# Kernel tuning notes

Measured on AMD Instinct MI355X. Metric: run time of the kernel, lower is better.

Reference implementation:

```python
import jax, jax.numpy as jnp
import numpy as np

T, H, E, K, I, S = 512, 1024, 32, 4, 512, 2048  # tokens, hidden, experts, top_k, moe_inter, shared_inter


def setup_inputs() -> dict:
    key = jax.random.key(0)
    ks = jax.random.split(key, 8)
    sc = 0.02
    return {
        "hidden_states": jax.random.normal(ks[0], (T, H), jnp.float32),
        "Wg": jax.random.normal(ks[1], (H, E + 1), jnp.float32) * sc,          # router gate + shared gate (merged)
        "W_gate": jax.random.normal(ks[2], (E, H, I), jnp.float32) * sc,        # per-expert gate proj
        "W_up": jax.random.normal(ks[3], (E, H, I), jnp.float32) * sc,          # per-expert up proj
        "W_down": jax.random.normal(ks[4], (E, I, H), jnp.float32) * sc,        # per-expert down proj
        "Ws_gate": jax.random.normal(ks[5], (H, S), jnp.float32) * sc,          # shared expert gate proj
        "Ws_up": jax.random.normal(ks[6], (H, S), jnp.float32) * sc,            # shared expert up proj
        "Ws_down": jax.random.normal(ks[7], (S, H), jnp.float32) * sc,          # shared expert down proj
    }


def reference(hidden_states, Wg, W_gate, W_up, W_down, Ws_gate, Ws_up, Ws_down):
    x = hidden_states  # [T, H]
    logits = x @ Wg                       # [T, E+1]
    router_logits = logits[:, :E]         # [T, E]
    shared_gate_logits = logits[:, E:]    # [T, 1]

    # top-k softmax routing with renormalization (renormalize=True)
    probs = jax.nn.softmax(router_logits, axis=-1)          # [T, E]
    topk_w, topk_idx = jax.lax.top_k(probs, K)               # [T, K]
    topk_w = topk_w / jnp.sum(topk_w, axis=-1, keepdims=True)
    combine = jnp.zeros((T, E), x.dtype).at[jnp.arange(T)[:, None], topk_idx].add(topk_w)  # [T, E]

    # routed experts: dense reference over all experts, combined by routing weights
    g = jnp.einsum("th,ehi->eti", x, W_gate)                 # [E, T, I]
    u = jnp.einsum("th,ehi->eti", x, W_up)                   # [E, T, I]
    h = jax.nn.silu(g) * u                                    # SiluAndMul
    y = jnp.einsum("eti,eih->eth", h, W_down)                # [E, T, H]
    routed = jnp.einsum("te,eth->th", combine, y)            # [T, H]

    # shared expert MLP + sigmoid shared-gate
    sh = (jax.nn.silu(x @ Ws_gate) * (x @ Ws_up)) @ Ws_down  # [T, H]
    shared = jax.nn.sigmoid(shared_gate_logits) * sh

    return shared + routed
```

## Files before the change

### kernel.cpp

```cpp
#include <hip/hip_runtime.h>
#include <hip/hip_bf16.h>

#define TT 512
#define HH 1024
#define EE 32
#define KK 4
#define II 512
#define SS 2048

using f32x4 = __attribute__((ext_vector_type(4))) float;
using s16x8 = __attribute__((ext_vector_type(8))) short;
using u32x4 = __attribute__((ext_vector_type(4))) unsigned;

__device__ __forceinline__ unsigned short f2bf(float f){
  unsigned int u = __builtin_bit_cast(unsigned int, f);
  u += 0x7fffu + ((u >> 16) & 1u);
  return (unsigned short)(u >> 16);
}
__device__ __forceinline__ unsigned pk2(float a, float b){
  return (unsigned)f2bf(a) | ((unsigned)f2bf(b) << 16);
}
__device__ __forceinline__ void barrier_lds(){
  asm volatile("s_waitcnt lgkmcnt(0)" ::: "memory");
  __builtin_amdgcn_s_barrier();
}

__global__ __launch_bounds__(64) void k_router(
    const float* __restrict__ x, const float* __restrict__ Wg,
    unsigned short* __restrict__ xb, int* __restrict__ topk_idx,
    float* __restrict__ topk_w, float* __restrict__ sig_gate){
  int t = blockIdx.x; int l = threadIdx.x;
  const float* xr = x + (size_t)t * HH;
  #pragma unroll
  for(int i=0;i<HH/64;i++){
    int h = l + 64*i;
    xb[(size_t)t*HH + h] = f2bf(xr[h]);
  }
  float acc0=0.f, acc1=0.f, acc2=0.f, acc3=0.f;
  if(l < EE+1){
    const float* wcol = Wg + l;
    for(int h=0; h<HH; h+=4){
      acc0 += xr[h]   * wcol[(size_t)h*(EE+1)];
      acc1 += xr[h+1] * wcol[(size_t)(h+1)*(EE+1)];
      acc2 += xr[h+2] * wcol[(size_t)(h+2)*(EE+1)];
      acc3 += xr[h+3] * wcol[(size_t)(h+3)*(EE+1)];
    }
  }
  __shared__ float lg[EE+1];
  if(l < EE+1) lg[l] = (acc0+acc1)+(acc2+acc3);
  __syncthreads();
  if(l == 0){
    float v[EE];
    #pragma unroll
    for(int i=0;i<EE;i++) v[i]=lg[i];
    int idx[KK]; float val[KK];
    #pragma unroll
    for(int k=0;k<KK;k++){
      float m=-1e30f; int mi=0;
      for(int i=0;i<EE;i++){ if(v[i]>m){ m=v[i]; mi=i; } }
      idx[k]=mi; val[k]=m; v[mi]=-1e30f;
    }
    float mx = val[0], s=0.f; float w[KK];
    #pragma unroll
    for(int k=0;k<KK;k++){ w[k]=__expf(val[k]-mx); s+=w[k]; }
    float inv = 1.f/s;
    #pragma unroll
    for(int k=0;k<KK;k++){ topk_idx[t*KK+k]=idx[k]; topk_w[t*KK+k]=w[k]*inv; }
    sig_gate[t] = 1.f/(1.f+__expf(-lg[EE]));
  }
}

__global__ __launch_bounds__(64) void k_build(
    const int* __restrict__ topk_idx, const float* __restrict__ topk_w,
    int* __restrict__ token_list, float* __restrict__ weight_list,
    int* __restrict__ counts){
  int e = blockIdx.x; int l = threadIdx.x;
  int cnt = 0;
  for(int c=0;c<TT;c+=64){
    int t = c + l;
    int kk = -1;
    #pragma unroll
    for(int k=0;k<KK;k++) if(topk_idx[t*KK+k]==e) kk=k;
    unsigned long long b = __ballot(kk>=0);
    int pre = __popcll(b & ((1ull<<l)-1ull));
    if(kk>=0){
      token_list[e*TT + cnt + pre] = t;
      weight_list[e*TT + cnt + pre] = topk_w[t*KK+kk];
    }
    cnt += __popcll(b);
  }
  if(l==0) counts[e]=cnt;
}

template<bool DUAL>
__device__ __forceinline__ void gemm64(
    const unsigned short* __restrict__ A0, bool va,
    const float* __restrict__ Gp, const float* __restrict__ Up,
    int ldb, int NK,
    f32x4* ag, f32x4* au,
    unsigned short* As, unsigned* Bg, unsigned* Bu, int tid){
  const int w = tid>>6, l = tid&63;
  const int ar = tid>>2, as_ = tid&3;
  const int m16 = tid&15, g2 = tid>>4;
  const int krow = 2*g2;
  const int kt = l>>4, mm = l&15;
  const unsigned swW = ((unsigned)((g2>>2)&3))<<3;
  const int wB  = g2*64 + ((4*m16) ^ (int)swW);
  const int aWr = ar*40 + as_*8;
  const int aRd = (w*16+mm)*40 + kt*8;
  const unsigned swR = ((unsigned)(kt&3))<<3;

  uint4 avA, avB;
  float4 gA0,gA1,uA0,uA1, gB0,gB1,uB0,uB1;

  auto loadBatch = [&](int b, uint4& av, float4& g0, float4& g1,
                       float4& u0, float4& u1){
    av = va ? *reinterpret_cast<const uint4*>(A0 + (size_t)b*32)
            : make_uint4(0,0,0,0);
    const float* p = Gp + (size_t)(b*32 + krow)*ldb;
    g0 = *reinterpret_cast<const float4*>(p);
    g1 = *reinterpret_cast<const float4*>(p + ldb);
    if(DUAL){
      const float* q = Up + (size_t)(b*32 + krow)*ldb;
      u0 = *reinterpret_cast<const float4*>(q);
      u1 = *reinterpret_cast<const float4*>(q + ldb);
    }
  };
  auto storeBatch = [&](int h, uint4 av, float4 g0, float4 g1,
                        float4 u0, float4 u1){
    *reinterpret_cast<uint4*>(As + (size_t)h*64*40 + aWr) = av;
    u32x4 vg; vg.x=pk2(g0.x,g1.x); vg.y=pk2(g0.y,g1.y);
    vg.z=pk2(g0.z,g1.z); vg.w=pk2(g0.w,g1.w);
    *reinterpret_cast<u32x4*>(Bg + (size_t)h*16*64 + wB) = vg;
    if(DUAL){
      u32x4 vu; vu.x=pk2(u0.x,u1.x); vu.y=pk2(u0.y,u1.y);
      vu.z=pk2(u0.z,u1.z); vu.w=pk2(u0.w,u1.w);
      *reinterpret_cast<u32x4*>(Bu + (size_t)h*16*64 + wB) = vu;
    }
  };
  auto compute = [&](int h){
    const unsigned* Bgh = Bg + (size_t)h*16*64;
    const unsigned* Buh = Bu + (size_t)h*16*64;
    s16x8 af = *reinterpret_cast<const s16x8*>(As + (size_t)h*64*40 + aRd);
    #pragma unroll
    for(int c=0;c<4;c++){
      int base = kt*4*64 + (((c*16+mm)) ^ (int)swR);
      u32x4 tg; tg.x=Bgh[base]; tg.y=Bgh[base+64];
      tg.z=Bgh[base+128]; tg.w=Bgh[base+192];
      s16x8 bg_ = __builtin_bit_cast(s16x8, tg);
      ag[c] = __builtin_amdgcn_mfma_f32_16x16x32_bf16(af, bg_, ag[c], 0,0,0);
      if(DUAL){
        u32x4 tu; tu.x=Buh[base]; tu.y=Buh[base+64];
        tu.z=Buh[base+128]; tu.w=Buh[base+192];
        s16x8 bu_ = __builtin_bit_cast(s16x8, tu);
        au[c] = __builtin_amdgcn_mfma_f32_16x16x32_bf16(af, bu_, au[c], 0,0,0);
      }
    }
  };

  loadBatch(0, avA, gA0,gA1, uA0,uA1);
  loadBatch(1, avB, gB0,gB1, uB0,uB1);
  storeBatch(0, avA, gA0,gA1, uA0,uA1);
  barrier_lds();
  for(int ks=0; ks<NK; ks+=2){
    const bool m2 = (ks+2 < NK), m3 = (ks+3 < NK);
    if(m2) loadBatch(ks+2, avA, gA0,gA1, uA0,uA1);
    compute(0);
    storeBatch(1, avB, gB0,gB1, uB0,uB1);
    barrier_lds();
    if(m3) loadBatch(ks+3, avB, gB0,gB1, uB0,uB1);
    compute(1);
    if(m2) storeBatch(0, avA, gA0,gA1, uA0,uA1);
    barrier_lds();
  }
}

__global__ __launch_bounds__(256) void k_gateup_all(
    const unsigned short* __restrict__ xb,
    const float* __restrict__ Wsg, const float* __restrict__ Wsu,
    unsigned short* __restrict__ Hs,
    const float* __restrict__ Wgate, const float* __restrict__ Wup,
    const int* __restrict__ token_list, const int* __restrict__ counts,
    unsigned short* __restrict__ hbuf){
  __shared__ __align__(16) unsigned short As[2*64*40];
  __shared__ __align__(16) unsigned Bg[2*16*64];
  __shared__ __align__(16) unsigned Bu[2*16*64];
  int tid = threadIdx.x, w = tid>>6, l = tid&63;
  int ar = tid>>2, as_ = tid&3, m16 = tid&15;
  int bid = blockIdx.x;
  f32x4 zero = {0.f,0.f,0.f,0.f};
  const int NSH = (TT/64)*(SS/64);

  if(bid < NSH){
    int n0 = (bid & 31) * 64;
    int r0 = (bid >> 5) * 64;
    f32x4 ag[4]={zero,zero,zero,zero}, au[4]={zero,zero,zero,zero};
    const unsigned short* A0 = xb + (size_t)(r0+ar)*HH + as_*8;
    const float* Gp = Wsg + n0 + 4*m16;
    const float* Up = Wsu + n0 + 4*m16;
    gemm64<true>(A0, true, Gp, Up, SS, HH/32, ag, au, As, Bg, Bu, tid);
    int mm = l&15, rb = r0 + w*16 + (l>>4)*4;
    #pragma unroll
    for(int c=0;c<4;c++){
      #pragma unroll
      for(int j=0;j<4;j++){
        float g = ag[c][j], u = au[c][j];
        Hs[(size_t)(rb+j)*SS + n0 + c*16 + mm] = f2bf(g*u/(1.f+__expf(-g)));
      }
    }
  } else {
    int b = bid - NSH;
    int e = b >> 3;
    int i0 = (b & 7) * 64;
    int cnt = counts[e]; if(cnt == 0) return;
    int off = 0;
    for(int i=0;i<e;i++) off += counts[i];
    const float* Gp0 = Wgate + (size_t)e*HH*II + i0 + 4*m16;
    const float* Up0 = Wup   + (size_t)e*HH*II + i0 + 4*m16;
    for(int rt=0; rt*64<cnt; rt++){
      int nv = cnt - rt*64; if(nv > 64) nv = 64;
      const int* rows = token_list + e*TT + rt*64;
      int arow = (ar < nv) ? rows[ar] : 0;
      bool va = ar < nv;
      f32x4 ag[4]={zero,zero,zero,zero}, au[4]={zero,zero,zero,zero};
      const unsigned short* A0 = xb + (size_t)arow*HH + as_*8;
      gemm64<true>(A0, va, Gp0, Up0, II, HH/32, ag, au, As, Bg, Bu, tid);
      int mm = l&15, rr0 = w*16 + (l>>4)*4;
      #pragma unroll
      for(int c=0;c<4;c++){
        #pragma unroll
        for(int j=0;j<4;j++){
          int rr = rr0 + j;
          if(rr < nv){
            float g = ag[c][j], u = au[c][j];
            hbuf[(size_t)(off+rt*64+rr)*II + i0 + c*16 + mm] =
                f2bf(g*u/(1.f+__expf(-g)));
          }
        }
      }
    }
  }
}

__global__ __launch_bounds__(256) void k_down_all(
    const unsigned short* __restrict__ Hsrc, const float* __restrict__ Wsd,
    const float* __restrict__ sig_gate,
    const unsigned short* __restrict__ hbuf, const float* __restrict__ Wdown,
    const int* __restrict__ token_list, const float* __restrict__ weight_list,
    const int* __restrict__ counts, float* __restrict__ out){
  __shared__ __align__(16) unsigned short As[2*64*40];
  __shared__ __align__(16) unsigned Bs[2*16*64];
  int tid = threadIdx.x, w = tid>>6, l = tid&63;
  int ar = tid>>2, as_ = tid&3, m16 = tid&15;
  int bid = blockIdx.x;
  f32x4 zero = {0.f,0.f,0.f,0.f};
  const int NSH = (TT/64)*(HH/64);

  if(bid < NSH){
    int n0 = (bid & 15) * 64;
    int r0 = (bid >> 4) * 64;
    f32x4 acc[4]={zero,zero,zero,zero};
    const unsigned short* A0 = Hsrc + (size_t)(r0+ar)*SS + as_*8;
    const float* Bp = Wsd + n0 + 4*m16;
    gemm64<false>(A0, true, Bp, Bp, HH, SS/32, acc, acc, As, Bs, Bs, tid);
    int mm = l&15, rb = r0 + w*16 + (l>>4)*4;
    #pragma unroll
    for(int c=0;c<4;c++){
      #pragma unroll
      for(int j=0;j<4;j++){
        atomicAdd(&out[(size_t)(rb+j)*HH + n0 + c*16 + mm],
                  sig_gate[rb+j]*acc[c][j]);
      }
    }
  } else {
    int b = bid - NSH;
    int e = b >> 4;
    int n0 = (b & 15) * 64;
    int cnt = counts[e]; if(cnt == 0) return;
    int off = 0;
    for(int i=0;i<e;i++) off += counts[i];
    const float* Bp = Wdown + (size_t)e*II*HH + n0 + 4*m16;
    for(int rt=0; rt*64<cnt; rt++){
      int nv = cnt - rt*64; if(nv > 64) nv = 64;
      bool va = ar < nv;
      f32x4 acc[4]={zero,zero,zero,zero};
      const unsigned short* A0 = hbuf + (size_t)(off+rt*64+ar)*II + as_*8;
      gemm64<false>(A0, va, Bp, Bp, HH, II/32, acc, acc, As, Bs, Bs, tid);
      int mm = l&15, rr0 = w*16 + (l>>4)*4;
      #pragma unroll
      for(int c=0;c<4;c++){
        #pragma unroll
        for(int j=0;j<4;j++){
          int rr = rr0 + j;
          if(rr < nv){
            int t = token_list[e*TT + rt*64 + rr];
            float wt = weight_list[e*TT + rt*64 + rr];
            atomicAdd(&out[(size_t)t*HH + n0 + c*16 + mm], wt*acc[c][j]);
          }
        }
      }
    }
  }
}

extern "C" void kernel_launch(void* const* d_in, const int* in_sizes, int n_in,
                              void* d_out, int out_size, void* d_ws, size_t ws_size,
                              hipStream_t stream) {
  const float* x     = (const float*)d_in[0];
  const float* Wg    = (const float*)d_in[1];
  const float* Wgate = (const float*)d_in[2];
  const float* Wup   = (const float*)d_in[3];
  const float* Wdown = (const float*)d_in[4];
  const float* Wsg   = (const float*)d_in[5];
  const float* Wsu   = (const float*)d_in[6];
  const float* Wsd   = (const float*)d_in[7];
  float* out = (float*)d_out;

  char* ws = (char*)d_ws;
  unsigned short* xb   = (unsigned short*)ws; ws += (size_t)TT*HH*2;
  unsigned short* Hs   = (unsigned short*)ws; ws += (size_t)TT*SS*2;
  unsigned short* hbuf = (unsigned short*)ws; ws += (size_t)(TT*KK+64)*II*2;
  int*   token_list  = (int*)ws;   ws += (size_t)EE*TT*4;
  float* weight_list = (float*)ws; ws += (size_t)EE*TT*4;
  int*   topk_idx    = (int*)ws;   ws += (size_t)TT*KK*4;
  float* topk_wq     = (float*)ws; ws += (size_t)TT*KK*4;
  int*   counts      = (int*)ws;   ws += 128;
  float* sig_gate    = (float*)ws; ws += (size_t)TT*4;

  hipMemsetAsync(d_out, 0, (size_t)TT*HH*4, stream);
  k_router<<<TT, 64, 0, stream>>>(x, Wg, xb, topk_idx, topk_wq, sig_gate);
  k_build<<<EE, 64, 0, stream>>>(topk_idx, topk_wq, token_list, weight_list, counts);
  k_gateup_all<<<(TT/64)*(SS/64) + EE*(II/64), 256, 0, stream>>>(
      xb, Wsg, Wsu, Hs, Wgate, Wup, token_list, counts, hbuf);
  k_down_all<<<(TT/64)*(HH/64) + EE*(HH/64), 256, 0, stream>>>(
      Hs, Wsd, sig_gate, hbuf, Wdown, token_list, weight_list, counts, out);
}
```

Baseline: 151.2 us.

## Load A tiles directly to LDS and deepen the GEMM pipeline to four stages

The shared GEMM helper now moves A-operand tiles straight from global memory into a 4-slot LDS ring using global_load_lds, with an XOR swizzle in place of padding. B weights are prefetched three stages ahead in registers, and sched_barrier keeps the schedule fixed across barriers. Invalid rows are clamped to a valid row instead of zero-filled, and launch_bounds(256,2) is added to encourage two blocks per CU. The aim is to hide global load latency and cut register round-trips for A, at the cost of more registers for the B prefetch slots. The loop assumes NK is a multiple of 4 and issues redundant clamped loads at the tail.

```diff
diff --git a/kernel.cpp b/kernel.cpp
--- a/kernel.cpp
+++ b/kernel.cpp
@@ -20,9 +20,12 @@
 __device__ __forceinline__ unsigned pk2(float a, float b){
   return (unsigned)f2bf(a) | ((unsigned)f2bf(b) << 16);
 }
-__device__ __forceinline__ void barrier_lds(){
-  asm volatile("s_waitcnt lgkmcnt(0)" ::: "memory");
-  __builtin_amdgcn_s_barrier();
+
+typedef __attribute__((address_space(1))) const unsigned GU;
+typedef __attribute__((address_space(3))) unsigned LU;
+
+__device__ __forceinline__ void gload16(const void* g, void* l){
+  __builtin_amdgcn_global_load_lds((GU*)g, (LU*)l, 16, 0, 0);
 }
 
 __global__ __launch_bounds__(64) void k_router(
@@ -92,101 +95,99 @@
   if(l==0) counts[e]=cnt;
 }
 
+
+#define ISSUE(S, SLOT) { \
+    int sc_ = ((S) < NK) ? (S) : (NK-1); \
+    gload16(Asrc + (size_t)sc_*32, Aw + (SLOT)*2048); \
+    const float* p_ = Gp + (size_t)(sc_*32 + krow)*ldb; \
+    bgs##SLOT##a = *reinterpret_cast<const float4*>(p_); \
+    bgs##SLOT##b = *reinterpret_cast<const float4*>(p_ + ldb); \
+    if(DUAL){ \
+      const float* q_ = Up + (size_t)(sc_*32 + krow)*ldb; \
+      bus##SLOT##a = *reinterpret_cast<const float4*>(q_); \
+      bus##SLOT##b = *reinterpret_cast<const float4*>(q_ + ldb); \
+    } }
+
+#define PACKB(SLOT, PAR) { \
+    u32x4 vg_; \
+    vg_.x = pk2(bgs##SLOT##a.x, bgs##SLOT##b.x); \
+    vg_.y = pk2(bgs##SLOT##a.y, bgs##SLOT##b.y); \
+    vg_.z = pk2(bgs##SLOT##a.z, bgs##SLOT##b.z); \
+    vg_.w = pk2(bgs##SLOT##a.w, bgs##SLOT##b.w); \
+    *reinterpret_cast<u32x4*>(Bg + (PAR)*1024 + wB) = vg_; \
+    if(DUAL){ u32x4 vu_; \
+      vu_.x = pk2(bus##SLOT##a.x, bus##SLOT##b.x); \
+      vu_.y = pk2(bus##SLOT##a.y, bus##SLOT##b.y); \
+      vu_.z = pk2(bus##SLOT##a.z, bus##SLOT##b.z); \
+      vu_.w = pk2(bus##SLOT##a.w, bus##SLOT##b.w); \
+      *reinterpret_cast<u32x4*>(Bu + (PAR)*1024 + wB) = vu_; } }
+
+#define COMPUTE(P) { \
+    s16x8 af_ = *reinterpret_cast<const s16x8*>(Al + (P)*2048 + aRd); \
+    const unsigned* Bgh_ = Bg + ((P)&1)*1024; \
+    const unsigned* Buh_ = Bu + ((P)&1)*1024; \
+    _Pragma("unroll") \
+    for(int c=0;c<4;c++){ \
+      int base_ = kt*256 + ((c*16+mm) ^ (int)swR); \
+      u32x4 tg_; tg_.x=Bgh_[base_]; tg_.y=Bgh_[base_+64]; \
+      tg_.z=Bgh_[base_+128]; tg_.w=Bgh_[base_+192]; \
+      ag[c] = __builtin_amdgcn_mfma_f32_16x16x32_bf16(af_, __builtin_bit_cast(s16x8, tg_), ag[c], 0,0,0); \
+      if(DUAL){ \
+        u32x4 tu_; tu_.x=Buh_[base_]; tu_.y=Buh_[base_+64]; \
+        tu_.z=Buh_[base_+128]; tu_.w=Buh_[base_+192]; \
+        au[c] = __builtin_amdgcn_mfma_f32_16x16x32_bf16(af_, __builtin_bit_cast(s16x8, tu_), au[c], 0,0,0); } } }
+
+#define BARR() { asm volatile("s_waitcnt lgkmcnt(0)" ::: "memory"); \
+    __builtin_amdgcn_s_barrier(); \
+    __builtin_amdgcn_sched_barrier(0); }
+
 template<bool DUAL>
-__device__ __forceinline__ void gemm64(
-    const unsigned short* __restrict__ A0, bool va,
+__device__ __forceinline__ void gemm64d(
+    const unsigned short* __restrict__ Asrc,
     const float* __restrict__ Gp, const float* __restrict__ Up,
     int ldb, int NK,
     f32x4* ag, f32x4* au,
-    unsigned short* As, unsigned* Bg, unsigned* Bu, int tid){
+    unsigned short* Al, unsigned* Bg, unsigned* Bu, int tid)
+{
   const int w = tid>>6, l = tid&63;
-  const int ar = tid>>2, as_ = tid&3;
   const int m16 = tid&15, g2 = tid>>4;
   const int krow = 2*g2;
   const int kt = l>>4, mm = l&15;
   const unsigned swW = ((unsigned)((g2>>2)&3))<<3;
-  const int wB  = g2*64 + ((4*m16) ^ (int)swW);
-  const int aWr = ar*40 + as_*8;
-  const int aRd = (w*16+mm)*40 + kt*8;
+  const int wB = g2*64 + ((4*m16) ^ (int)swW);
+  const int arow = w*16 + mm;
+  const int aRd = arow*32 + ((kt ^ ((arow>>1)&3))<<3);
   const unsigned swR = ((unsigned)(kt&3))<<3;
-
-  uint4 avA, avB;
-  float4 gA0,gA1,uA0,uA1, gB0,gB1,uB0,uB1;
-
-  auto loadBatch = [&](int b, uint4& av, float4& g0, float4& g1,
-                       float4& u0, float4& u1){
-    av = va ? *reinterpret_cast<const uint4*>(A0 + (size_t)b*32)
-            : make_uint4(0,0,0,0);
-    const float* p = Gp + (size_t)(b*32 + krow)*ldb;
-    g0 = *reinterpret_cast<const float4*>(p);
-    g1 = *reinterpret_cast<const float4*>(p + ldb);
-    if(DUAL){
-      const float* q = Up + (size_t)(b*32 + krow)*ldb;
-      u0 = *reinterpret_cast<const float4*>(q);
-      u1 = *reinterpret_cast<const float4*>(q + ldb);
-    }
-  };
-  auto storeBatch = [&](int h, uint4 av, float4 g0, float4 g1,
-                        float4 u0, float4 u1){
-    *reinterpret_cast<uint4*>(As + (size_t)h*64*40 + aWr) = av;
-    u32x4 vg; vg.x=pk2(g0.x,g1.x); vg.y=pk2(g0.y,g1.y);
-    vg.z=pk2(g0.z,g1.z); vg.w=pk2(g0.w,g1.w);
-    *reinterpret_cast<u32x4*>(Bg + (size_t)h*16*64 + wB) = vg;
-    if(DUAL){
-      u32x4 vu; vu.x=pk2(u0.x,u1.x); vu.y=pk2(u0.y,u1.y);
-      vu.z=pk2(u0.z,u1.z); vu.w=pk2(u0.w,u1.w);
-      *reinterpret_cast<u32x4*>(Bu + (size_t)h*16*64 + wB) = vu;
-    }
-  };
-  auto compute = [&](int h){
-    const unsigned* Bgh = Bg + (size_t)h*16*64;
-    const unsigned* Buh = Bu + (size_t)h*16*64;
-    s16x8 af = *reinterpret_cast<const s16x8*>(As + (size_t)h*64*40 + aRd);
-    #pragma unroll
-    for(int c=0;c<4;c++){
-      int base = kt*4*64 + (((c*16+mm)) ^ (int)swR);
-      u32x4 tg; tg.x=Bgh[base]; tg.y=Bgh[base+64];
-      tg.z=Bgh[base+128]; tg.w=Bgh[base+192];
-      s16x8 bg_ = __builtin_bit_cast(s16x8, tg);
-      ag[c] = __builtin_amdgcn_mfma_f32_16x16x32_bf16(af, bg_, ag[c], 0,0,0);
-      if(DUAL){
-        u32x4 tu; tu.x=Buh[base]; tu.y=Buh[base+64];
-        tu.z=Buh[base+128]; tu.w=Buh[base+192];
-        s16x8 bu_ = __builtin_bit_cast(s16x8, tu);
-        au[c] = __builtin_amdgcn_mfma_f32_16x16x32_bf16(af, bu_, au[c], 0,0,0);
-      }
-    }
-  };
-
-  loadBatch(0, avA, gA0,gA1, uA0,uA1);
-  loadBatch(1, avB, gB0,gB1, uB0,uB1);
-  storeBatch(0, avA, gA0,gA1, uA0,uA1);
-  barrier_lds();
-  for(int ks=0; ks<NK; ks+=2){
-    const bool m2 = (ks+2 < NK), m3 = (ks+3 < NK);
-    if(m2) loadBatch(ks+2, avA, gA0,gA1, uA0,uA1);
-    compute(0);
-    storeBatch(1, avB, gB0,gB1, uB0,uB1);
-    barrier_lds();
-    if(m3) loadBatch(ks+3, avB, gB0,gB1, uB0,uB1);
-    compute(1);
-    if(m2) storeBatch(0, avA, gA0,gA1, uA0,uA1);
-    barrier_lds();
-  }
-}
-
-__global__ __launch_bounds__(256) void k_gateup_all(
+  unsigned short* Aw = Al + w*512;
+
+  float4 bgs0a,bgs0b,bgs1a,bgs1b,bgs2a,bgs2b,bgs3a,bgs3b;
+  float4 bus0a,bus0b,bus1a,bus1b,bus2a,bus2b,bus3a,bus3b;
+
+  ISSUE(0,0) ISSUE(1,1) ISSUE(2,2)
+  PACKB(0,0)
+  BARR()
+  for(int ks=0; ks<NK; ks+=4){
+    ISSUE(ks+3,3) COMPUTE(0) PACKB(1,1) BARR()
+    ISSUE(ks+4,0) COMPUTE(1) PACKB(2,0) BARR()
+    ISSUE(ks+5,1) COMPUTE(2) PACKB(3,1) BARR()
+    ISSUE(ks+6,2) COMPUTE(3) PACKB(0,0) BARR()
+  }
+}
+
+__global__ __launch_bounds__(256, 2) void k_gateup_all(
     const unsigned short* __restrict__ xb,
     const float* __restrict__ Wsg, const float* __restrict__ Wsu,
     unsigned short* __restrict__ Hs,
     const float* __restrict__ Wgate, const float* __restrict__ Wup,
     const int* __restrict__ token_list, const int* __restrict__ counts,
     unsigned short* __restrict__ hbuf){
-  __shared__ __align__(16) unsigned short As[2*64*40];
-  __shared__ __align__(16) unsigned Bg[2*16*64];
-  __shared__ __align__(16) unsigned Bu[2*16*64];
+  __shared__ __align__(16) unsigned short Albuf[4*64*32];
+  __shared__ __align__(16) unsigned Bgbuf[2*16*64];
+  __shared__ __align__(16) unsigned Bubuf[2*16*64];
   int tid = threadIdx.x, w = tid>>6, l = tid&63;
-  int ar = tid>>2, as_ = tid&3, m16 = tid&15;
+  int m16 = tid&15;
+  const int r_lds = w*16 + (l>>2);
+  const int sseg  = (l&3) ^ ((r_lds>>1)&3);
   int bid = blockIdx.x;
   f32x4 zero = {0.f,0.f,0.f,0.f};
   const int NSH = (TT/64)*(SS/64);
@@ -195,10 +196,10 @@
     int n0 = (bid & 31) * 64;
     int r0 = (bid >> 5) * 64;
     f32x4 ag[4]={zero,zero,zero,zero}, au[4]={zero,zero,zero,zero};
-    const unsigned short* A0 = xb + (size_t)(r0+ar)*HH + as_*8;
+    const unsigned short* Asrc = xb + (size_t)(r0 + r_lds)*HH + sseg*8;
     const float* Gp = Wsg + n0 + 4*m16;
     const float* Up = Wsu + n0 + 4*m16;
-    gemm64<true>(A0, true, Gp, Up, SS, HH/32, ag, au, As, Bg, Bu, tid);
+    gemm64d<true>(Asrc, Gp, Up, SS, HH/32, ag, au, Albuf, Bgbuf, Bubuf, tid);
     int mm = l&15, rb = r0 + w*16 + (l>>4)*4;
     #pragma unroll
     for(int c=0;c<4;c++){
@@ -215,16 +216,16 @@
     int cnt = counts[e]; if(cnt == 0) return;
     int off = 0;
     for(int i=0;i<e;i++) off += counts[i];
-    const float* Gp0 = Wgate + (size_t)e*HH*II + i0 + 4*m16;
-    const float* Up0 = Wup   + (size_t)e*HH*II + i0 + 4*m16;
+    const float* Gp = Wgate + (size_t)e*HH*II + i0 + 4*m16;
+    const float* Up = Wup   + (size_t)e*HH*II + i0 + 4*m16;
     for(int rt=0; rt*64<cnt; rt++){
       int nv = cnt - rt*64; if(nv > 64) nv = 64;
       const int* rows = token_list + e*TT + rt*64;
-      int arow = (ar < nv) ? rows[ar] : 0;
-      bool va = ar < nv;
+      int rr_ = r_lds < nv ? r_lds : nv-1;
+      int rowg = rows[rr_];
       f32x4 ag[4]={zero,zero,zero,zero}, au[4]={zero,zero,zero,zero};
-      const unsigned short* A0 = xb + (size_t)arow*HH + as_*8;
-      gemm64<true>(A0, va, Gp0, Up0, II, HH/32, ag, au, As, Bg, Bu, tid);
+      const unsigned short* Asrc = xb + (size_t)rowg*HH + sseg*8;
+      gemm64d<true>(Asrc, Gp, Up, II, HH/32, ag, au, Albuf, Bgbuf, Bubuf, tid);
       int mm = l&15, rr0 = w*16 + (l>>4)*4;
       #pragma unroll
       for(int c=0;c<4;c++){
@@ -242,16 +243,18 @@
   }
 }
 
-__global__ __launch_bounds__(256) void k_down_all(
+__global__ __launch_bounds__(256, 2) void k_down_all(
     const unsigned short* __restrict__ Hsrc, const float* __restrict__ Wsd,
     const float* __restrict__ sig_gate,
     const unsigned short* __restrict__ hbuf, const float* __restrict__ Wdown,
     const int* __restrict__ token_list, const float* __restrict__ weight_list,
     const int* __restrict__ counts, float* __restrict__ out){
-  __shared__ __align__(16) unsigned short As[2*64*40];
-  __shared__ __align__(16) unsigned Bs[2*16*64];
+  __shared__ __align__(16) unsigned short Albuf[4*64*32];
+  __shared__ __align__(16) unsigned Bsbuf[2*16*64];
   int tid = threadIdx.x, w = tid>>6, l = tid&63;
-  int ar = tid>>2, as_ = tid&3, m16 = tid&15;
+  int m16 = tid&15;
+  const int r_lds = w*16 + (l>>2);
+  const int sseg  = (l&3) ^ ((r_lds>>1)&3);
   int bid = blockIdx.x;
   f32x4 zero = {0.f,0.f,0.f,0.f};
   const int NSH = (TT/64)*(HH/64);
@@ -260,9 +263,9 @@
     int n0 = (bid & 15) * 64;
     int r0 = (bid >> 4) * 64;
     f32x4 acc[4]={zero,zero,zero,zero};
-    const unsigned short* A0 = Hsrc + (size_t)(r0+ar)*SS + as_*8;
+    const unsigned short* Asrc = Hsrc + (size_t)(r0 + r_lds)*SS + sseg*8;
     const float* Bp = Wsd + n0 + 4*m16;
-    gemm64<false>(A0, true, Bp, Bp, HH, SS/32, acc, acc, As, Bs, Bs, tid);
+    gemm64d<false>(Asrc, Bp, Bp, HH, SS/32, acc, acc, Albuf, Bsbuf, Bsbuf, tid);
     int mm = l&15, rb = r0 + w*16 + (l>>4)*4;
     #pragma unroll
     for(int c=0;c<4;c++){
@@ -282,10 +285,11 @@
     const float* Bp = Wdown + (size_t)e*II*HH + n0 + 4*m16;
     for(int rt=0; rt*64<cnt; rt++){
       int nv = cnt - rt*64; if(nv > 64) nv = 64;
-      bool va = ar < nv;
+      int rr_ = r_lds < nv ? r_lds : nv-1;
       f32x4 acc[4]={zero,zero,zero,zero};
-      const unsigned short* A0 = hbuf + (size_t)(off+rt*64+ar)*II + as_*8;
-      gemm64<false>(A0, va, Bp, Bp, HH, II/32, acc, acc, As, Bs, Bs, tid);
+      const unsigned short* Asrc =
+          hbuf + (size_t)(off+rt*64+rr_)*II + sseg*8;
+      gemm64d<false>(Asrc, Bp, Bp, HH, II/32, acc, acc, Albuf, Bsbuf, Bsbuf, tid);
       int mm = l&15, rr0 = w*16 + (l>>4)*4;
       #pragma unroll
       for(int c=0;c<4;c++){
```

New measurement: 158.9 us. +5.1%, slower.
